# Kernel optimization log

Hardware: AMD Instinct MI355X
Metric: run time of the kernel (lower is better)

Reference implementation:

```python
import jax, jax.numpy as jnp
import numpy as np

V, E, H, C = 30000, 128, 256, 9  # vocab, embed dim, lstm hidden, num tags
B, S = 64, 512


def setup_inputs() -> dict:
    key = jax.random.key(0)
    ks = jax.random.split(key, 16)
    rn = lambda k, shape: jax.random.normal(k, shape, jnp.float32) * 0.1
    return {
        "token_ids": jax.random.randint(ks[0], (B, S), 0, V),
        "labels": jax.random.randint(ks[1], (B, S), 0, C),
        "attention_masks": jnp.ones((B, S), jnp.int32),
        "emb": rn(ks[2], (V, E)),
        # layer 0: input E; layer 1: input 2H. dim 0 = direction (fwd, bwd)
        "w_ih0": rn(ks[3], (2, 4 * H, E)),
        "w_hh0": rn(ks[4], (2, 4 * H, H)),
        "b_ih0": rn(ks[5], (2, 4 * H)),
        "b_hh0": rn(ks[6], (2, 4 * H)),
        "w_ih1": rn(ks[7], (2, 4 * H, 2 * H)),
        "w_hh1": rn(ks[8], (2, 4 * H, H)),
        "b_ih1": rn(ks[9], (2, 4 * H)),
        "b_hh1": rn(ks[10], (2, 4 * H)),
        "cls_w": rn(ks[11], (C, 2 * H)),
        "cls_b": rn(ks[12], (C,)),
        "start_trans": rn(ks[13], (C,)),
        "end_trans": rn(ks[14], (C,)),
        "trans": rn(ks[15], (C, C)),
    }


def _lstm_dir(x, w_ih, w_hh, b_ih, b_hh, reverse):
    # x: [B,S,in] -> [B,S,H]; gate order i,f,g,o as in torch
    Bq = x.shape[0]
    Hq = w_hh.shape[1]
    xg = jnp.einsum('bsi,gi->bsg', x, w_ih) + b_ih  # [B,S,4H]

    def step(carry, xg_t):
        h, c = carry
        g = xg_t + h @ w_hh.T + b_hh
        i, f, gg, o = jnp.split(g, 4, axis=-1)
        c = jax.nn.sigmoid(f) * c + jax.nn.sigmoid(i) * jnp.tanh(gg)
        h = jax.nn.sigmoid(o) * jnp.tanh(c)
        return (h, c), h

    init = (jnp.zeros((Bq, Hq), x.dtype), jnp.zeros((Bq, Hq), x.dtype))
    _, hs = jax.lax.scan(step, init, jnp.swapaxes(xg, 0, 1), reverse=reverse)
    return jnp.swapaxes(hs, 0, 1)


def _bilstm_layer(x, w_ih, w_hh, b_ih, b_hh):
    fwd = _lstm_dir(x, w_ih[0], w_hh[0], b_ih[0], b_hh[0], False)
    bwd = _lstm_dir(x, w_ih[1], w_hh[1], b_ih[1], b_hh[1], True)
    return jnp.concatenate([fwd, bwd], axis=-1)


def _crf_llh(em, tags, mask, start, end, trans):
    # torchcrf log-likelihood; em [B,S,C], tags [B,S], mask [B,S]
    m = mask.astype(em.dtype)
    em_tag = jnp.take_along_axis(em, tags[..., None], axis=2)[..., 0]  # [B,S]
    tr = trans[tags[:, :-1], tags[:, 1:]]  # [B,S-1]
    num = start[tags[:, 0]] + em_tag[:, 0] + jnp.sum(m[:, 1:] * (tr + em_tag[:, 1:]), axis=1)
    last_idx = jnp.sum(mask, axis=1).astype(jnp.int32) - 1
    last_tag = jnp.take_along_axis(tags, last_idx[:, None], axis=1)[:, 0]
    num = num + end[last_tag]

    alpha0 = start[None, :] + em[:, 0]  # [B,C]

    def step(alpha, xs):
        em_t, m_t = xs
        nxt = jax.nn.logsumexp(alpha[:, :, None] + trans[None] + em_t[:, None, :], axis=1)
        return jnp.where(m_t[:, None] > 0, nxt, alpha), None

    xs = (jnp.swapaxes(em[:, 1:], 0, 1), jnp.swapaxes(m[:, 1:], 0, 1))
    alpha, _ = jax.lax.scan(step, alpha0, xs)
    den = jax.nn.logsumexp(alpha + end[None, :], axis=1)
    return num - den


def _viterbi(em, mask, start, end, trans):
    Cq = em.shape[2]
    m = mask > 0
    score0 = start[None, :] + em[:, 0]
    idc = jnp.arange(Cq, dtype=jnp.int32)

    def step(score, xs):
        em_t, m_t = xs
        brd = score[:, :, None] + trans[None]  # [B,C_prev,C_next]
        best_prev = jnp.argmax(brd, axis=1).astype(jnp.int32)
        nxt = jnp.max(brd, axis=1) + em_t
        new = jnp.where(m_t[:, None], nxt, score)
        bp = jnp.where(m_t[:, None], best_prev, idc[None, :])  # self-pointer past seq end
        return new, bp

    xs = (jnp.swapaxes(em[:, 1:], 0, 1), jnp.swapaxes(m[:, 1:], 0, 1))
    score, hist = jax.lax.scan(step, score0, xs)  # hist: [S-1,B,C]
    last = jnp.argmax(score + end[None, :], axis=1).astype(jnp.int32)

    def back(tag, bp_t):
        prev = jnp.take_along_axis(bp_t, tag[:, None], axis=1)[:, 0]
        return prev, prev

    _, prevs = jax.lax.scan(back, last, hist, reverse=True)  # [S-1,B]
    return jnp.concatenate([jnp.swapaxes(prevs, 0, 1), last[:, None]], axis=1)  # [B,S]


def reference(token_ids, labels, attention_masks, emb, w_ih0, w_hh0, b_ih0, b_hh0,
              w_ih1, w_hh1, b_ih1, b_hh1, cls_w, cls_b, start_trans, end_trans, trans):
    x = emb[token_ids]  # [B,S,E]
    h = _bilstm_layer(x, w_ih0, w_hh0, b_ih0, b_hh0)  # [B,S,2H] (eval mode: no dropout)
    h = _bilstm_layer(h, w_ih1, w_hh1, b_ih1, b_hh1)
    emissions = h @ cls_w.T + cls_b  # [B,S,C]
    llh = _crf_llh(emissions, labels, attention_masks, start_trans, end_trans, trans)
    loss = -jnp.mean(llh)  # reduction='mean', negated
    tags = _viterbi(emissions, attention_masks, start_trans, end_trans, trans)
    return (loss, tags)
```

## Files before the change

kernel.cpp:

```cpp
#include <hip/hip_runtime.h>
#include <math.h>

#define BB 64
#define SS 512
#define HH 256
#define NC 9
#define G4 1024
#define TCLOG 7
#define TC 128
#define NCH (SS / TC)
#define VV 30000

#define KLQ 9

typedef _Float16 half2v __attribute__((ext_vector_type(2)));

__device__ __forceinline__ float sigf(float x) {
    return 1.0f / (1.0f + __expf(-x));
}
__device__ __forceinline__ float tanhfast(float x) {
    float a = fabsf(x);
    float e = __expf(-2.0f * a);
    float t = (1.0f - e) / (1.0f + e);
    return copysignf(t, x);
}
__device__ __forceinline__ int dot16q(uint4 w, uint4 h, int acc) {
    acc = __builtin_amdgcn_sdot4((int)w.x, (int)h.x, acc, false);
    acc = __builtin_amdgcn_sdot4((int)w.y, (int)h.y, acc, false);
    acc = __builtin_amdgcn_sdot4((int)w.z, (int)h.z, acc, false);
    acc = __builtin_amdgcn_sdot4((int)w.w, (int)h.w, acc, false);
    return acc;
}
__device__ __forceinline__ ushort f16b(float x) {
    return __builtin_bit_cast(ushort, (_Float16)x);
}

struct GJob {
    const unsigned char* A;
    const int*   tok;
    const unsigned char* W;
    const float* sw;
    const float* swA;
    const float* bias;
    ushort*      out;
    int tb, ts, is8, pad;
};
struct SJob {
    const ushort* xgF; const ushort* xgB;
    const uint*  wTq; const float* swf; const float* bhh2;
    ushort* hout; unsigned char* hout8; float* state;
    int doW8, tbF, tbB, doInit;
};
struct MegaP {
    SJob s;
    GJob g[4];
    int nScan, nGemm;
};

__device__ __forceinline__ int pad4(int r) { return r + (r >> 3); }

__device__ void gemm8_dev(unsigned char* sm, const GJob& G, int bx, int by) {
    uint4* As = (uint4*)sm;
    uint4* Bs = As + 144;
    const int tid = threadIdx.x;
    const int m0 = bx * 128, n0 = by * 128;
    const int lr = tid & 127;
    const int lpad = lr + (lr >> 3);
    const bool isA = tid < 128, isB = (tid >= 128 && tid < 256);
    const int tcc = (m0 + lr) & (TC - 1);
    const int bb  = (m0 + lr) >> TCLOG;
    const int tglob = G.tb + G.ts * tcc;
    const long arow = (long)bb * SS + tglob;
    const uint4* Ap = isA ? (const uint4*)(G.A + arow * 512) : nullptr;
    const uint4* Wp = isB ? (const uint4*)(G.W + (long)(n0 + lr) * 512) : nullptr;
    const int tr = tid >> 5, tn = tid & 31;

    int acc[4][4];
    #pragma unroll
    for (int i = 0; i < 4; i++)
        #pragma unroll
        for (int j = 0; j < 4; j++) acc[i][j] = 0;

    #pragma unroll 1
    for (int k0 = 0; k0 < 32; k0++) {
        if (isA) As[lpad] = Ap[k0];
        else if (isB) Bs[lpad] = Wp[k0];
        __syncthreads();
        uint4 a[4], w[4];
        #pragma unroll
        for (int i = 0; i < 4; i++) {
            a[i] = As[pad4(tr * 4 + i)];
            w[i] = Bs[pad4(tn * 4 + i)];
        }
        #pragma unroll
        for (int i = 0; i < 4; i++)
            #pragma unroll
            for (int j = 0; j < 4; j++)
                acc[i][j] = dot16q(w[j], a[i], acc[i][j]);
        __syncthreads();
    }

    #pragma unroll
    for (int i = 0; i < 4; i++) {
        ushort4 o;
        #pragma unroll
        for (int j = 0; j < 4; j++) {
            float r = fmaf((float)acc[i][j], G.sw[n0 + tn * 4 + j], G.bias[n0 + tn * 4 + j]);
            ((ushort*)&o)[j] = f16b(r);
        }
        *(ushort4*)(G.out + (long)(m0 + tr * 4 + i) * G4 + n0 + tn * 4) = o;
    }
}

__device__ void gemm8e_dev(unsigned char* sm, const GJob& G, int bx, int by) {
    uint4* As = (uint4*)sm;
    uint4* Bs = As + 144;
    const int tid = threadIdx.x;
    const int m0 = bx * 128, n0 = by * 128;
    const int lr = tid & 127;
    const int lpad = lr + (lr >> 3);
    const bool isA = tid < 128, isB = (tid >= 128 && tid < 256);
    const int tcc = (m0 + lr) & (TC - 1);
    const int bb  = (m0 + lr) >> TCLOG;
    const int tglob = G.tb + G.ts * tcc;
    const long arow = (long)bb * SS + tglob;
    const uint4* Ap = isA ? (const uint4*)(G.A + (long)G.tok[arow] * 128) : nullptr;
    const uint4* Wp = isB ? (const uint4*)(G.W + (long)(n0 + lr) * 128) : nullptr;
    const int tr = tid >> 5, tn = tid & 31;

    int acc[4][4];
    #pragma unroll
    for (int i = 0; i < 4; i++)
        #pragma unroll
        for (int j = 0; j < 4; j++) acc[i][j] = 0;

    #pragma unroll 1
    for (int k0 = 0; k0 < 8; k0++) {
        if (isA) As[lpad] = Ap[k0];
        else if (isB) Bs[lpad] = Wp[k0];
        __syncthreads();
        uint4 a[4], w[4];
        #pragma unroll
        for (int i = 0; i < 4; i++) {
            a[i] = As[pad4(tr * 4 + i)];
            w[i] = Bs[pad4(tn * 4 + i)];
        }
        #pragma unroll
        for (int i = 0; i < 4; i++)
            #pragma unroll
            for (int j = 0; j < 4; j++)
                acc[i][j] = dot16q(w[j], a[i], acc[i][j]);
        __syncthreads();
    }

    float sA[4];
    #pragma unroll
    for (int i = 0; i < 4; i++) {
        const int m = m0 + tr * 4 + i;
        const int tcc_i = m & (TC - 1);
        const int bb_i  = m >> TCLOG;
        const long ar = (long)bb_i * SS + G.tb + G.ts * tcc_i;
        sA[i] = G.swA[G.tok[ar]];
    }
    float sW[4], bs[4];
    #pragma unroll
    for (int j = 0; j < 4; j++) {
        sW[j] = G.sw[n0 + tn * 4 + j];
        bs[j] = G.bias[n0 + tn * 4 + j];
    }
    #pragma unroll
    for (int i = 0; i < 4; i++) {
        ushort4 o;
        #pragma unroll
        for (int j = 0; j < 4; j++) {
            float r = fmaf((float)acc[i][j] * sA[i], sW[j], bs[j]);
            ((ushort*)&o)[j] = f16b(r);
        }
        *(ushort4*)(G.out + (long)(m0 + tr * 4 + i) * G4 + n0 + tn * 4) = o;
    }
}

__device__ void scan_dev(unsigned char* sm, const SJob& S, int b, int d) {
    const int j = threadIdx.x;
    const ushort* xg = (d ? S.xgB : S.xgF) + (long)b * TC * G4 + j;
    const uint4* wTd = (const uint4*)S.wTq + (long)d * 16 * 1024;

    uint4* lwq = (uint4*)sm;
    float* gl  = (float*)(sm + 147456);
    uint*  hq  = (uint*)(sm + 147456 + 4096);

    #pragma unroll
    for (int kc = 0; kc < KLQ; kc++)
        lwq[kc * 1024 + j] = wTd[(long)kc * 1024 + j];

    const float bj  = S.bhh2[d * G4 + j];
    const float scl = S.swf[d * G4 + j];
    float c_reg = 0.f, h_reg = 0.f;
    if (j < HH) {
        if (!S.doInit) {
            h_reg = S.state[((d * BB + b) * 2 + 0) * HH + j];
            c_reg = S.state[((d * BB + b) * 2 + 1) * HH + j];
        }
        ((char*)hq)[j] = (char)__float2int_rn(h_reg * 127.f);
    }
    __syncthreads();

    #pragma unroll 1
    for (int tc = 0; tc < TC; ++tc) {
        const int rb = tc & 1;
        const uint4* hc = (const uint4*)(hq + rb * 64);
        int isum = 0;
        #pragma unroll
        for (int kc = 0; kc < KLQ; kc++)
            isum = dot16q(lwq[kc * 1024 + j], hc[kc], isum);
        #pragma unroll
        for (int kc = KLQ; kc < 16; kc++)
            isum = dot16q(wTd[(long)kc * 1024 + j], hc[kc], isum);

        float xv = (float)__builtin_bit_cast(_Float16, xg[(long)tc * G4]);
        gl[j] = fmaf((float)isum, scl, xv + bj);
        __syncthreads();
        if (j < HH) {
            float gi = gl[j], gf = gl[j + 256], gg = gl[j + 512], go = gl[j + 768];
            c_reg = sigf(gf) * c_reg + sigf(gi) * tanhfast(gg);
            float h = sigf(go) * tanhfast(c_reg);
            h_reg = h;
            int qh = __float2int_rn(h * 127.f);
            ((char*)(hq + (rb ^ 1) * 64))[j] = (char)qh;
            const int t = d ? (S.tbB - tc) : (S.tbF + tc);
            if (S.doW8) S.hout8[((long)(b * SS + t)) * 512 + d * HH + j] = (unsigned char)(char)qh;
            else        S.hout [((long)(b * SS + t)) * 512 + d * HH + j] = f16b(h);
        }
        __syncthreads();
    }

    if (j < HH) {
        S.state[((d * BB + b) * 2 + 0) * HH + j] = h_reg;
        S.state[((d * BB + b) * 2 + 1) * HH + j] = c_reg;
    }
}

__global__ __launch_bounds__(1024, 4) void mega(MegaP p) {
    __shared__ __align__(16) unsigned char sm[152064];
    const int blk = blockIdx.x;
    if (blk < p.nScan * 128) {
        const int local = blk & 127;
        scan_dev(sm, p.s, local & 63, local >> 6);
    } else {
        const int gb = blk - p.nScan * 128;
        const int job = gb >> 9, t = gb & 511;
        const GJob& G = p.g[job];
        if (G.is8 == 1) gemm8_dev(sm, G, t & 63, t >> 6);
        else            gemm8e_dev(sm, G, t & 63, t >> 6);
    }
}

__global__ void quant_whh(const float* __restrict__ whh, uint* __restrict__ wTq,
                          float* __restrict__ swf) {
    const int row = blockIdx.x;
    const int t = threadIdx.x;
    float4 v = *(const float4*)(whh + (long)row * 256 + t * 4);
    float mx = fmaxf(fmaxf(fabsf(v.x), fabsf(v.y)), fmaxf(fabsf(v.z), fabsf(v.w)));
    #pragma unroll
    for (int o = 32; o > 0; o >>= 1) mx = fmaxf(mx, __shfl_xor(mx, o));
    float inv = (mx > 0.f) ? 127.f / mx : 0.f;
    int q0 = (int)rintf(v.x * inv) & 255;
    int q1 = (int)rintf(v.y * inv) & 255;
    int q2 = (int)rintf(v.z * inv) & 255;
    int q3 = (int)rintf(v.w * inv) & 255;
    uint u = (uint)q0 | ((uint)q1 << 8) | ((uint)q2 << 16) | ((uint)q3 << 24);
    const int dir = row >> 10, j = row & 1023;
    const int kc = t >> 2, l4 = t & 3;
    wTq[(((long)(dir * 16 + kc) * 1024 + j) << 2) + l4] = u;
    if (t == 0) swf[row] = (mx > 0.f) ? (mx / 127.f) * (1.f / 127.f) : 0.f;
}

template <int NP>
__global__ void quant_rows(const float* __restrict__ in, unsigned char* __restrict__ out,
                           float* __restrict__ sc, int mode) {
    const int row = blockIdx.x;
    const int t = threadIdx.x;
    const int K = NP * 64;
    const float* src = in + (long)row * K + t * NP;
    float v[NP];
    float mx = 0.f;
    #pragma unroll
    for (int i = 0; i < NP; i++) { v[i] = src[i]; mx = fmaxf(mx, fabsf(v[i])); }
    #pragma unroll
    for (int o = 32; o > 0; o >>= 1) mx = fmaxf(mx, __shfl_xor(mx, o));
    float inv = (mx > 0.f) ? 127.f / mx : 0.f;
    unsigned char q[NP];
    #pragma unroll
    for (int i = 0; i < NP; i++) q[i] = (unsigned char)((int)rintf(v[i] * inv) & 255);
    unsigned char* dst = out + (long)row * K + t * NP;
    if (NP == 2) {
        *(ushort*)dst = *(ushort*)q;
    } else {
        *(uint*)dst = *(uint*)q;
        *(uint*)(dst + 4) = *(uint*)(q + 4);
    }
    if (t == 0) sc[row] = (mx <= 0.f) ? 0.f
                        : (mode == 0 ? mx / 127.f : mx / (127.f * 127.f));
}

__global__ __launch_bounds__(256) void emissions_k16(
    const ushort* __restrict__ h1, const float* __restrict__ clsw,
    const float* __restrict__ clsb, float* __restrict__ em)
{
    long u = (long)blockIdx.x * 256 + threadIdx.x;
    if (u >= (long)BB * SS * NC) return;
    int c = (int)(u % NC);
    long m = u / NC;
    const uint* hr = (const uint*)(h1 + m * 512);
    const float2* wr = (const float2*)(clsw + (long)c * 512);
    float s0 = 0, s1 = 0;
    #pragma unroll 8
    for (int q = 0; q < 256; q += 2) {
        half2v h0 = __builtin_bit_cast(half2v, hr[q]);
        half2v h1v = __builtin_bit_cast(half2v, hr[q + 1]);
        float2 w0 = wr[q], w1 = wr[q + 1];
        s0 += (float)h0.x * w0.x + (float)h0.y * w0.y;
        s1 += (float)h1v.x * w1.x + (float)h1v.y * w1.y;
    }
    em[u] = s0 + s1 + clsb[c];
}

__global__ __launch_bounds__(64) void crf_llh(
    const float* __restrict__ em, const int* __restrict__ labels,
    const int* __restrict__ mask, const float* __restrict__ start,
    const float* __restrict__ endt, const float* __restrict__ trans,
    float* __restrict__ llh)
{
    int b = blockIdx.x, j = threadIdx.x;
    bool act = j < NC;
    float tcol[NC];
    #pragma unroll
    for (int i = 0; i < NC; i++) tcol[i] = act ? trans[i * NC + j] : 0.f;
    const float* emb_ = em + (long)b * SS * NC;
    const int* lb = labels + b * SS;
    const int* mk = mask + b * SS;
    float alpha = act ? (start[j] + emb_[j]) : -1e30f;

    float num = 0.f;
    int msum = 0;
    for (int t = j; t < SS; t += 64) msum += (mk[t] != 0);
    for (int t = 1 + j; t < SS; t += 64) {
        float m = (float)mk[t];
        num += m * (trans[lb[t - 1] * NC + lb[t]] + emb_[t * NC + lb[t]]);
    }
    for (int o = 32; o > 0; o >>= 1) {
        num  += __shfl_down(num, o);
        msum += __shfl_down(msum, o);
    }
    msum = __shfl(msum, 0);

    for (int t = 1; t < SS; t++) {
        int m = mk[t];
        float emj = act ? emb_[t * NC + j] : 0.f;
        float v[NC];
        float mx = -1e30f;
        #pragma unroll
        for (int i = 0; i < NC; i++) {
            v[i] = __shfl(alpha, i) + tcol[i];
            mx = fmaxf(mx, v[i]);
        }
        float sum = 0.f;
        #pragma unroll
        for (int i = 0; i < NC; i++) sum += __expf(v[i] - mx);
        float nxt = mx + __logf(sum) + emj;
        if (m > 0 && act) alpha = nxt;
    }
    float fin = act ? alpha + endt[j] : -1e30f;
    float mx = -1e30f;
    #pragma unroll
    for (int i = 0; i < NC; i++) mx = fmaxf(mx, __shfl(fin, i));
    float s = 0.f;
    #pragma unroll
    for (int i = 0; i < NC; i++) s += __expf(__shfl(fin, i) - mx);
    float den = mx + __logf(s);
    if (j == 0) {
        int last_idx = msum - 1;
        float numer = num + start[lb[0]] + emb_[lb[0]] + endt[lb[last_idx]];
        llh[b] = numer - den;
    }
}

__global__ __launch_bounds__(64) void loss_k(const float* __restrict__ llh, float* __restrict__ out) {
    int j = threadIdx.x;
    float v = llh[j];
    for (int o = 32; o > 0; o >>= 1) v += __shfl_down(v, o);
    if (j == 0) out[0] = -v / 64.0f;
}

__global__ __launch_bounds__(64) void viterbi_k(
    const float* __restrict__ em, const int* __restrict__ mask,
    const float* __restrict__ start, const float* __restrict__ endt,
    const float* __restrict__ trans, float* __restrict__ outp)
{
    int b = blockIdx.x, j = threadIdx.x;
    bool act = j < NC;
    __shared__ unsigned char bp[SS][NC];
    float tcol[NC];
    #pragma unroll
    for (int i = 0; i < NC; i++) tcol[i] = act ? trans[i * NC + j] : 0.f;
    const float* emb_ = em + (long)b * SS * NC;
    const int* mk = mask + b * SS;
    float score = act ? (start[j] + emb_[j]) : -1e30f;

    for (int t = 1; t < SS; t++) {
        float best = 0.f;
        int bi = 0;
        #pragma unroll
        for (int i = 0; i < NC; i++) {
            float vv = __shfl(score, i) + tcol[i];
            if (i == 0 || vv > best) { best = vv; bi = i; }
        }
        int m = mk[t];
        float nxt = best + (act ? emb_[t * NC + j] : 0.f);
        if (act) {
            if (m > 0) { score = nxt; bp[t][j] = (unsigned char)bi; }
            else       { bp[t][j] = (unsigned char)j; }
        }
    }
    float fin = act ? score + endt[j] : -1e30f;
    float bestf = 0.f;
    int last = 0;
    #pragma unroll
    for (int i = 0; i < NC; i++) {
        float vv = __shfl(fin, i);
        if (i == 0 || vv > bestf) { bestf = vv; last = i; }
    }
    __syncthreads();
    if (j == 0) {
        int cur = last;
        outp[1 + (long)b * SS + (SS - 1)] = (float)cur;
        for (int t = SS - 1; t >= 1; t--) {
            cur = bp[t][cur];
            outp[1 + (long)b * SS + (t - 1)] = (float)cur;
        }
    }
}

extern "C" void kernel_launch(void* const* d_in, const int* in_sizes, int n_in,
                              void* d_out, int out_size, void* d_ws, size_t ws_size,
                              hipStream_t stream) {
    const int*   tok    = (const int*)d_in[0];
    const int*   lab    = (const int*)d_in[1];
    const int*   msk    = (const int*)d_in[2];
    const float* emb    = (const float*)d_in[3];
    const float* w_ih0  = (const float*)d_in[4];
    const float* w_hh0  = (const float*)d_in[5];
    const float* b_ih0  = (const float*)d_in[6];
    const float* b_hh0  = (const float*)d_in[7];
    const float* w_ih1  = (const float*)d_in[8];
    const float* w_hh1  = (const float*)d_in[9];
    const float* b_ih1  = (const float*)d_in[10];
    const float* b_hh1  = (const float*)d_in[11];
    const float* clsw   = (const float*)d_in[12];
    const float* clsb   = (const float*)d_in[13];
    const float* startt = (const float*)d_in[14];
    const float* endt   = (const float*)d_in[15];
    const float* transm = (const float*)d_in[16];
    float* out = (float*)d_out;

    size_t nH8  = (size_t)BB * SS * 512 / 4;
    size_t nHh  = (size_t)BB * SS * 512 / 2;
    size_t xgHalf = (size_t)BB * TC * G4;
    size_t nXGb = xgHalf * 2 / 2;
    size_t nWQ  = (size_t)2 * 16 * 1024 * 4;
    size_t nSW  = (size_t)2 * 1024;
    size_t nWQ1 = (size_t)2048 * 512 / 4;
    size_t nWQ0 = (size_t)2048 * 128 / 4;
    size_t nE8  = (size_t)VV * 128 / 4;
    size_t nEM  = (size_t)BB * SS * NC;
    size_t nST  = (size_t)2 * BB * 2 * HH;

    float* H08f = (float*)d_ws;
    float* H1f  = H08f + nH8;
    float* XG0a = H1f + nHh;
    float* XG0b = XG0a + nXGb;
    float* XG1a = XG0b + nXGb;
    float* XG1b = XG1a + nXGb;
    float* WQ0  = XG1b + nXGb;
    float* WQ1w = WQ0 + nWQ;
    float* SW0  = WQ1w + nWQ;
    float* SW1  = SW0 + nSW;
    float* WQI1 = SW1 + nSW;
    float* SWI1 = WQI1 + nWQ1;
    float* WQI0 = SWI1 + 2048;
    float* SWI0 = WQI0 + nWQ0;
    float* EMB8 = SWI0 + 2048;
    float* SA   = EMB8 + nE8;
    float* EM   = SA + VV;
    float* ST0  = EM + nEM;
    float* ST1  = ST0 + nST;
    float* LLH  = ST1 + nST;

    unsigned char* H08   = (unsigned char*)H08f;
    ushort*        H1h   = (ushort*)H1f;
    unsigned char* WQI1b = (unsigned char*)WQI1;
    unsigned char* WQI0b = (unsigned char*)WQI0;
    unsigned char* EMB8b = (unsigned char*)EMB8;
    ushort* XG0[2] = {(ushort*)XG0a, (ushort*)XG0b};
    ushort* XG1[2] = {(ushort*)XG1a, (ushort*)XG1b};

    quant_whh<<<2048, 64, 0, stream>>>(w_hh0, (uint*)WQ0, SW0);
    quant_whh<<<2048, 64, 0, stream>>>(w_hh1, (uint*)WQ1w, SW1);
    quant_rows<8><<<2048, 64, 0, stream>>>(w_ih1, WQI1b, SWI1, 1);
    quant_rows<2><<<2048, 64, 0, stream>>>(w_ih0, WQI0b, SWI0, 0);
    quant_rows<2><<<VV, 64, 0, stream>>>(emb, EMB8b, SA, 0);

    auto g0 = [&](int c, int dd) {
        GJob g{};
        g.A = EMB8b; g.tok = tok;
        g.W = WQI0b + (size_t)dd * 1024 * 128;
        g.sw = SWI0 + dd * 1024; g.swA = SA; g.bias = b_ih0 + dd * 1024;
        g.out = XG0[c & 1] + (size_t)dd * xgHalf;
        g.tb = dd ? (SS - 1 - c * TC) : (c * TC);
        g.ts = dd ? -1 : 1;
        g.is8 = 2;
        return g;
    };
    auto g8 = [&](int c, int dd) {
        GJob g{};
        g.A = H08; g.tok = nullptr;
        g.W = WQI1b + (size_t)dd * 1024 * 512;
        g.sw = SWI1 + dd * 1024; g.swA = nullptr; g.bias = b_ih1 + dd * 1024;
        g.out = XG1[c & 1] + (size_t)dd * xgHalf;
        g.tb = dd ? (SS - 1 - c * TC) : (c * TC);
        g.ts = dd ? -1 : 1;
        g.is8 = 1;
        return g;
    };
    auto sj = [&](int layer, int c) {
        SJob s{};
        ushort* xgb = layer ? XG1[c & 1] : XG0[c & 1];
        s.xgF = xgb; s.xgB = xgb + xgHalf;
        s.wTq = (const uint*)(layer ? WQ1w : WQ0);
        s.swf = layer ? SW1 : SW0;
        s.bhh2 = layer ? b_hh1 : b_hh0;
        s.hout = H1h; s.hout8 = H08;
        s.doW8 = layer ? 0 : 1;
        s.state = layer ? ST1 : ST0;
        s.tbF = c * TC; s.tbB = SS - 1 - c * TC;
        s.doInit = (c == 0);
        return s;
    };
    auto launch = [&](int nS, SJob s, GJob* gj, int nG) {
        MegaP p{};
        p.s = s;
        for (int i = 0; i < nG; i++) p.g[i] = gj[i];
        p.nScan = nS; p.nGemm = nG;
        mega<<<nS * 128 + nG * 512, 1024, 0, stream>>>(p);
    };

    { GJob j2[2] = {g0(0, 0), g0(0, 1)};          launch(0, SJob{}, j2, 2); }
    { GJob j2[2] = {g0(1, 0), g0(1, 1)};          launch(1, sj(0, 0), j2, 2); }
    { GJob j2[2] = {g0(2, 0), g0(2, 1)};          launch(1, sj(0, 1), j2, 2); }
    { GJob j4[4] = {g0(3, 0), g0(3, 1), g8(0, 0), g8(0, 1)};
                                                   launch(1, sj(0, 2), j4, 4); }
    { GJob j2[2] = {g8(1, 0), g8(1, 1)};          launch(1, sj(0, 3), j2, 2); }
    {                                              launch(1, sj(1, 0), nullptr, 0); }
    { GJob j2[2] = {g8(2, 0), g8(2, 1)};          launch(1, sj(1, 1), j2, 2); }
    { GJob j2[2] = {g8(3, 0), g8(3, 1)};          launch(1, sj(1, 2), j2, 2); }
    {                                              launch(1, sj(1, 3), nullptr, 0); }

    emissions_k16<<<((BB * SS * NC) + 255) / 256, 256, 0, stream>>>(H1h, clsw, clsb, EM);
    crf_llh<<<BB, 64, 0, stream>>>(EM, lab, msk, startt, endt, transm, LLH);
    loss_k<<<1, 64, 0, stream>>>(LLH, out);
    viterbi_k<<<BB, 64, 0, stream>>>(EM, msk, startt, endt, transm, out);
}
```

Before: 2.042 ms.

## Replace chunked mega-kernel pipeline with whole-sequence GEMM then full LSTM scan

Removes the chunked schedule in which each mega-kernel launch overlapped one 128-step scan chunk with the input-projection GEMM for the next chunk. Instead, each layer now runs one full GEMM over all timesteps, followed by a single scan kernel covering all 512 steps, which drops the per-chunk state save and restore and the extra launches. The CRF likelihood and Viterbi kernels are merged into one launch with 2*BB blocks. The cost is that GEMM work no longer overlaps with the latency-bound scan, and a full-size gate buffer is needed.

```diff
diff --git a/kernel.cpp b/kernel.cpp
--- a/kernel.cpp
+++ b/kernel.cpp
@@ -6,9 +6,6 @@
 #define HH 256
 #define NC 9
 #define G4 1024
-#define TCLOG 7
-#define TC 128
-#define NCH (SS / TC)
 #define VV 30000
 
 #define KLQ 9
@@ -34,226 +31,7 @@
 __device__ __forceinline__ ushort f16b(float x) {
     return __builtin_bit_cast(ushort, (_Float16)x);
 }
-
-struct GJob {
-    const unsigned char* A;
-    const int*   tok;
-    const unsigned char* W;
-    const float* sw;
-    const float* swA;
-    const float* bias;
-    ushort*      out;
-    int tb, ts, is8, pad;
-};
-struct SJob {
-    const ushort* xgF; const ushort* xgB;
-    const uint*  wTq; const float* swf; const float* bhh2;
-    ushort* hout; unsigned char* hout8; float* state;
-    int doW8, tbF, tbB, doInit;
-};
-struct MegaP {
-    SJob s;
-    GJob g[4];
-    int nScan, nGemm;
-};
-
 __device__ __forceinline__ int pad4(int r) { return r + (r >> 3); }
-
-__device__ void gemm8_dev(unsigned char* sm, const GJob& G, int bx, int by) {
-    uint4* As = (uint4*)sm;
-    uint4* Bs = As + 144;
-    const int tid = threadIdx.x;
-    const int m0 = bx * 128, n0 = by * 128;
-    const int lr = tid & 127;
-    const int lpad = lr + (lr >> 3);
-    const bool isA = tid < 128, isB = (tid >= 128 && tid < 256);
-    const int tcc = (m0 + lr) & (TC - 1);
-    const int bb  = (m0 + lr) >> TCLOG;
-    const int tglob = G.tb + G.ts * tcc;
-    const long arow = (long)bb * SS + tglob;
-    const uint4* Ap = isA ? (const uint4*)(G.A + arow * 512) : nullptr;
-    const uint4* Wp = isB ? (const uint4*)(G.W + (long)(n0 + lr) * 512) : nullptr;
-    const int tr = tid >> 5, tn = tid & 31;
-
-    int acc[4][4];
-    #pragma unroll
-    for (int i = 0; i < 4; i++)
-        #pragma unroll
-        for (int j = 0; j < 4; j++) acc[i][j] = 0;
-
-    #pragma unroll 1
-    for (int k0 = 0; k0 < 32; k0++) {
-        if (isA) As[lpad] = Ap[k0];
-        else if (isB) Bs[lpad] = Wp[k0];
-        __syncthreads();
-        uint4 a[4], w[4];
-        #pragma unroll
-        for (int i = 0; i < 4; i++) {
-            a[i] = As[pad4(tr * 4 + i)];
-            w[i] = Bs[pad4(tn * 4 + i)];
-        }
-        #pragma unroll
-        for (int i = 0; i < 4; i++)
-            #pragma unroll
-            for (int j = 0; j < 4; j++)
-                acc[i][j] = dot16q(w[j], a[i], acc[i][j]);
-        __syncthreads();
-    }
-
-    #pragma unroll
-    for (int i = 0; i < 4; i++) {
-        ushort4 o;
-        #pragma unroll
-        for (int j = 0; j < 4; j++) {
-            float r = fmaf((float)acc[i][j], G.sw[n0 + tn * 4 + j], G.bias[n0 + tn * 4 + j]);
-            ((ushort*)&o)[j] = f16b(r);
-        }
-        *(ushort4*)(G.out + (long)(m0 + tr * 4 + i) * G4 + n0 + tn * 4) = o;
-    }
-}
-
-__device__ void gemm8e_dev(unsigned char* sm, const GJob& G, int bx, int by) {
-    uint4* As = (uint4*)sm;
-    uint4* Bs = As + 144;
-    const int tid = threadIdx.x;
-    const int m0 = bx * 128, n0 = by * 128;
-    const int lr = tid & 127;
-    const int lpad = lr + (lr >> 3);
-    const bool isA = tid < 128, isB = (tid >= 128 && tid < 256);
-    const int tcc = (m0 + lr) & (TC - 1);
-    const int bb  = (m0 + lr) >> TCLOG;
-    const int tglob = G.tb + G.ts * tcc;
-    const long arow = (long)bb * SS + tglob;
-    const uint4* Ap = isA ? (const uint4*)(G.A + (long)G.tok[arow] * 128) : nullptr;
-    const uint4* Wp = isB ? (const uint4*)(G.W + (long)(n0 + lr) * 128) : nullptr;
-    const int tr = tid >> 5, tn = tid & 31;
-
-    int acc[4][4];
-    #pragma unroll
-    for (int i = 0; i < 4; i++)
-        #pragma unroll
-        for (int j = 0; j < 4; j++) acc[i][j] = 0;
-
-    #pragma unroll 1
-    for (int k0 = 0; k0 < 8; k0++) {
-        if (isA) As[lpad] = Ap[k0];
-        else if (isB) Bs[lpad] = Wp[k0];
-        __syncthreads();
-        uint4 a[4], w[4];
-        #pragma unroll
-        for (int i = 0; i < 4; i++) {
-            a[i] = As[pad4(tr * 4 + i)];
-            w[i] = Bs[pad4(tn * 4 + i)];
-        }
-        #pragma unroll
-        for (int i = 0; i < 4; i++)
-            #pragma unroll
-            for (int j = 0; j < 4; j++)
-                acc[i][j] = dot16q(w[j], a[i], acc[i][j]);
-        __syncthreads();
-    }
-
-    float sA[4];
-    #pragma unroll
-    for (int i = 0; i < 4; i++) {
-        const int m = m0 + tr * 4 + i;
-        const int tcc_i = m & (TC - 1);
-        const int bb_i  = m >> TCLOG;
-        const long ar = (long)bb_i * SS + G.tb + G.ts * tcc_i;
-        sA[i] = G.swA[G.tok[ar]];
-    }
-    float sW[4], bs[4];
-    #pragma unroll
-    for (int j = 0; j < 4; j++) {
-        sW[j] = G.sw[n0 + tn * 4 + j];
-        bs[j] = G.bias[n0 + tn * 4 + j];
-    }
-    #pragma unroll
-    for (int i = 0; i < 4; i++) {
-        ushort4 o;
-        #pragma unroll
-        for (int j = 0; j < 4; j++) {
-            float r = fmaf((float)acc[i][j] * sA[i], sW[j], bs[j]);
-            ((ushort*)&o)[j] = f16b(r);
-        }
-        *(ushort4*)(G.out + (long)(m0 + tr * 4 + i) * G4 + n0 + tn * 4) = o;
-    }
-}
-
-__device__ void scan_dev(unsigned char* sm, const SJob& S, int b, int d) {
-    const int j = threadIdx.x;
-    const ushort* xg = (d ? S.xgB : S.xgF) + (long)b * TC * G4 + j;
-    const uint4* wTd = (const uint4*)S.wTq + (long)d * 16 * 1024;
-
-    uint4* lwq = (uint4*)sm;
-    float* gl  = (float*)(sm + 147456);
-    uint*  hq  = (uint*)(sm + 147456 + 4096);
-
-    #pragma unroll
-    for (int kc = 0; kc < KLQ; kc++)
-        lwq[kc * 1024 + j] = wTd[(long)kc * 1024 + j];
-
-    const float bj  = S.bhh2[d * G4 + j];
-    const float scl = S.swf[d * G4 + j];
-    float c_reg = 0.f, h_reg = 0.f;
-    if (j < HH) {
-        if (!S.doInit) {
-            h_reg = S.state[((d * BB + b) * 2 + 0) * HH + j];
-            c_reg = S.state[((d * BB + b) * 2 + 1) * HH + j];
-        }
-        ((char*)hq)[j] = (char)__float2int_rn(h_reg * 127.f);
-    }
-    __syncthreads();
-
-    #pragma unroll 1
-    for (int tc = 0; tc < TC; ++tc) {
-        const int rb = tc & 1;
-        const uint4* hc = (const uint4*)(hq + rb * 64);
-        int isum = 0;
-        #pragma unroll
-        for (int kc = 0; kc < KLQ; kc++)
-            isum = dot16q(lwq[kc * 1024 + j], hc[kc], isum);
-        #pragma unroll
-        for (int kc = KLQ; kc < 16; kc++)
-            isum = dot16q(wTd[(long)kc * 1024 + j], hc[kc], isum);
-
-        float xv = (float)__builtin_bit_cast(_Float16, xg[(long)tc * G4]);
-        gl[j] = fmaf((float)isum, scl, xv + bj);
-        __syncthreads();
-        if (j < HH) {
-            float gi = gl[j], gf = gl[j + 256], gg = gl[j + 512], go = gl[j + 768];
-            c_reg = sigf(gf) * c_reg + sigf(gi) * tanhfast(gg);
-            float h = sigf(go) * tanhfast(c_reg);
-            h_reg = h;
-            int qh = __float2int_rn(h * 127.f);
-            ((char*)(hq + (rb ^ 1) * 64))[j] = (char)qh;
-            const int t = d ? (S.tbB - tc) : (S.tbF + tc);
-            if (S.doW8) S.hout8[((long)(b * SS + t)) * 512 + d * HH + j] = (unsigned char)(char)qh;
-            else        S.hout [((long)(b * SS + t)) * 512 + d * HH + j] = f16b(h);
-        }
-        __syncthreads();
-    }
-
-    if (j < HH) {
-        S.state[((d * BB + b) * 2 + 0) * HH + j] = h_reg;
-        S.state[((d * BB + b) * 2 + 1) * HH + j] = c_reg;
-    }
-}
-
-__global__ __launch_bounds__(1024, 4) void mega(MegaP p) {
-    __shared__ __align__(16) unsigned char sm[152064];
-    const int blk = blockIdx.x;
-    if (blk < p.nScan * 128) {
-        const int local = blk & 127;
-        scan_dev(sm, p.s, local & 63, local >> 6);
-    } else {
-        const int gb = blk - p.nScan * 128;
-        const int job = gb >> 9, t = gb & 511;
-        const GJob& G = p.g[job];
-        if (G.is8 == 1) gemm8_dev(sm, G, t & 63, t >> 6);
-        else            gemm8e_dev(sm, G, t & 63, t >> 6);
-    }
-}
 
 __global__ void quant_whh(const float* __restrict__ whh, uint* __restrict__ wTq,
                           float* __restrict__ swf) {
@@ -301,6 +79,197 @@
     }
     if (t == 0) sc[row] = (mx <= 0.f) ? 0.f
                         : (mode == 0 ? mx / 127.f : mx / (127.f * 127.f));
+}
+
+__global__ __launch_bounds__(1024, 2) void gemm8e_k(
+    const unsigned char* __restrict__ A8,
+    const int* __restrict__ tok,
+    const unsigned char* __restrict__ Wq,
+    const float* __restrict__ sw,
+    const float* __restrict__ swA,
+    const float* __restrict__ bias,
+    ushort* __restrict__ xg)
+{
+    __shared__ uint4 As[144], Bs[144];
+    const int tid = threadIdx.x;
+    const int m0 = blockIdx.x * 128;
+    const int n0 = blockIdx.y * 128;
+    const int d  = blockIdx.z;
+    const unsigned char* W = Wq + (size_t)d * 1024 * 128;
+    const float* swd = sw + d * 1024;
+    const float* bd  = bias + d * 1024;
+    ushort* outd = xg + (size_t)d * BB * SS * G4;
+
+    const int lr = tid & 127;
+    const int lpad = lr + (lr >> 3);
+    const bool isA = tid < 128, isB = (tid >= 128 && tid < 256);
+    const uint4* Ap = isA ? (const uint4*)(A8 + (long)tok[m0 + lr] * 128) : nullptr;
+    const uint4* Wp = isB ? (const uint4*)(W + (long)(n0 + lr) * 128) : nullptr;
+    const int tr = tid >> 5, tn = tid & 31;
+
+    int acc[4][4];
+    #pragma unroll
+    for (int i = 0; i < 4; i++)
+        #pragma unroll
+        for (int j = 0; j < 4; j++) acc[i][j] = 0;
+
+    #pragma unroll 1
+    for (int k0 = 0; k0 < 8; k0++) {
+        if (isA) As[lpad] = Ap[k0];
+        else if (isB) Bs[lpad] = Wp[k0];
+        __syncthreads();
+        uint4 a[4], w[4];
+        #pragma unroll
+        for (int i = 0; i < 4; i++) {
+            a[i] = As[pad4(tr * 4 + i)];
+            w[i] = Bs[pad4(tn * 4 + i)];
+        }
+        #pragma unroll
+        for (int i = 0; i < 4; i++)
+            #pragma unroll
+            for (int j = 0; j < 4; j++)
+                acc[i][j] = dot16q(w[j], a[i], acc[i][j]);
+        __syncthreads();
+    }
+
+    float sA[4];
+    #pragma unroll
+    for (int i = 0; i < 4; i++) sA[i] = swA[tok[m0 + tr * 4 + i]];
+    float sW[4], bs[4];
+    #pragma unroll
+    for (int j = 0; j < 4; j++) {
+        sW[j] = swd[n0 + tn * 4 + j];
+        bs[j] = bd[n0 + tn * 4 + j];
+    }
+    #pragma unroll
+    for (int i = 0; i < 4; i++) {
+        ushort4 o;
+        #pragma unroll
+        for (int j = 0; j < 4; j++) {
+            float r = fmaf((float)acc[i][j] * sA[i], sW[j], bs[j]);
+            ((ushort*)&o)[j] = f16b(r);
+        }
+        *(ushort4*)(outd + (long)(m0 + tr * 4 + i) * G4 + n0 + tn * 4) = o;
+    }
+}
+
+__global__ __launch_bounds__(1024, 2) void gemm8_k(
+    const unsigned char* __restrict__ A8,
+    const unsigned char* __restrict__ Wq,
+    const float* __restrict__ sw,
+    const float* __restrict__ bias,
+    ushort* __restrict__ xg)
+{
+    __shared__ uint4 As[144], Bs[144];
+    const int tid = threadIdx.x;
+    const int m0 = blockIdx.x * 128;
+    const int n0 = blockIdx.y * 128;
+    const int d  = blockIdx.z;
+    const unsigned char* W = Wq + (size_t)d * 1024 * 512;
+    const float* swd = sw + d * 1024;
+    const float* bd  = bias + d * 1024;
+    ushort* outd = xg + (size_t)d * BB * SS * G4;
+
+    const int lr = tid & 127;
+    const int lpad = lr + (lr >> 3);
+    const bool isA = tid < 128, isB = (tid >= 128 && tid < 256);
+    const uint4* Ap = isA ? (const uint4*)(A8 + (long)(m0 + lr) * 512) : nullptr;
+    const uint4* Wp = isB ? (const uint4*)(W + (long)(n0 + lr) * 512) : nullptr;
+    const int tr = tid >> 5, tn = tid & 31;
+
+    int acc[4][4];
+    #pragma unroll
+    for (int i = 0; i < 4; i++)
+        #pragma unroll
+        for (int j = 0; j < 4; j++) acc[i][j] = 0;
+
+    #pragma unroll 1
+    for (int k0 = 0; k0 < 32; k0++) {
+        if (isA) As[lpad] = Ap[k0];
+        else if (isB) Bs[lpad] = Wp[k0];
+        __syncthreads();
+        uint4 a[4], w[4];
+        #pragma unroll
+        for (int i = 0; i < 4; i++) {
+            a[i] = As[pad4(tr * 4 + i)];
+            w[i] = Bs[pad4(tn * 4 + i)];
+        }
+        #pragma unroll
+        for (int i = 0; i < 4; i++)
+            #pragma unroll
+            for (int j = 0; j < 4; j++)
+                acc[i][j] = dot16q(w[j], a[i], acc[i][j]);
+        __syncthreads();
+    }
+
+    #pragma unroll
+    for (int i = 0; i < 4; i++) {
+        ushort4 o;
+        #pragma unroll
+        for (int j = 0; j < 4; j++) {
+            float r = fmaf((float)acc[i][j], swd[n0 + tn * 4 + j], bd[n0 + tn * 4 + j]);
+            ((ushort*)&o)[j] = f16b(r);
+        }
+        *(ushort4*)(outd + (long)(m0 + tr * 4 + i) * G4 + n0 + tn * 4) = o;
+    }
+}
+
+__global__ __launch_bounds__(1024, 4) void lstm_qscan(
+    const ushort* __restrict__ xg,
+    const uint* __restrict__ wTq,
+    const float* __restrict__ swf,
+    const float* __restrict__ bhh2,
+    ushort* __restrict__ hout,
+    unsigned char* __restrict__ hout8,
+    int doW8)
+{
+    const int b = blockIdx.x;
+    const int d = blockIdx.y;
+    const int j = threadIdx.x;
+    const ushort* xgd = xg + ((size_t)d * BB * SS + (size_t)b * SS) * G4 + j;
+    const uint4* wTd = (const uint4*)wTq + (long)d * 16 * 1024;
+
+    __shared__ __align__(16) uint hq[2][64];
+    __shared__ float gl[G4];
+    __shared__ uint4 lwq[KLQ * 1024];
+
+    #pragma unroll
+    for (int kc = 0; kc < KLQ; kc++)
+        lwq[kc * 1024 + j] = wTd[(long)kc * 1024 + j];
+
+    const float bj  = bhh2[d * G4 + j];
+    const float scl = swf[d * G4 + j];
+    float c_reg = 0.f;
+    if (j < HH) ((char*)hq[0])[j] = 0;
+    __syncthreads();
+
+    #pragma unroll 1
+    for (int tc = 0; tc < SS; ++tc) {
+        const int rb = tc & 1;
+        const int t = d ? (SS - 1 - tc) : tc;
+        const uint4* hc = (const uint4*)hq[rb];
+        int isum = 0;
+        #pragma unroll
+        for (int kc = 0; kc < KLQ; kc++)
+            isum = dot16q(lwq[kc * 1024 + j], hc[kc], isum);
+        #pragma unroll
+        for (int kc = KLQ; kc < 16; kc++)
+            isum = dot16q(wTd[(long)kc * 1024 + j], hc[kc], isum);
+
+        float xv = (float)__builtin_bit_cast(_Float16, xgd[(long)t * G4]);
+        gl[j] = fmaf((float)isum, scl, xv + bj);
+        __syncthreads();
+        if (j < HH) {
+            float gi = gl[j], gf = gl[j + 256], gg = gl[j + 512], go = gl[j + 768];
+            c_reg = sigf(gf) * c_reg + sigf(gi) * tanhfast(gg);
+            float h = sigf(go) * tanhfast(c_reg);
+            int qh = __float2int_rn(h * 127.f);
+            ((char*)hq[rb ^ 1])[j] = (char)qh;
+            if (doW8) hout8[((long)(b * SS + t)) * 512 + d * HH + j] = (unsigned char)(char)qh;
+            else      hout [((long)(b * SS + t)) * 512 + d * HH + j] = f16b(h);
+        }
+        __syncthreads();
+    }
 }
 
 __global__ __launch_bounds__(256) void emissions_k16(
@@ -325,63 +294,108 @@
     em[u] = s0 + s1 + clsb[c];
 }
 
-__global__ __launch_bounds__(64) void crf_llh(
+__global__ __launch_bounds__(64) void crfvit_k(
     const float* __restrict__ em, const int* __restrict__ labels,
     const int* __restrict__ mask, const float* __restrict__ start,
     const float* __restrict__ endt, const float* __restrict__ trans,
-    float* __restrict__ llh)
+    float* __restrict__ llh, float* __restrict__ outp)
 {
-    int b = blockIdx.x, j = threadIdx.x;
-    bool act = j < NC;
-    float tcol[NC];
-    #pragma unroll
-    for (int i = 0; i < NC; i++) tcol[i] = act ? trans[i * NC + j] : 0.f;
-    const float* emb_ = em + (long)b * SS * NC;
-    const int* lb = labels + b * SS;
-    const int* mk = mask + b * SS;
-    float alpha = act ? (start[j] + emb_[j]) : -1e30f;
-
-    float num = 0.f;
-    int msum = 0;
-    for (int t = j; t < SS; t += 64) msum += (mk[t] != 0);
-    for (int t = 1 + j; t < SS; t += 64) {
-        float m = (float)mk[t];
-        num += m * (trans[lb[t - 1] * NC + lb[t]] + emb_[t * NC + lb[t]]);
-    }
-    for (int o = 32; o > 0; o >>= 1) {
-        num  += __shfl_down(num, o);
-        msum += __shfl_down(msum, o);
-    }
-    msum = __shfl(msum, 0);
-
-    for (int t = 1; t < SS; t++) {
-        int m = mk[t];
-        float emj = act ? emb_[t * NC + j] : 0.f;
-        float v[NC];
+    __shared__ unsigned char bp[SS][NC];
+    const int j = threadIdx.x;
+    const bool act = j < NC;
+    if (blockIdx.x < BB) {
+        const int b = blockIdx.x;
+        float tcol[NC];
+        #pragma unroll
+        for (int i = 0; i < NC; i++) tcol[i] = act ? trans[i * NC + j] : 0.f;
+        const float* emb_ = em + (long)b * SS * NC;
+        const int* lb = labels + b * SS;
+        const int* mk = mask + b * SS;
+        float alpha = act ? (start[j] + emb_[j]) : -1e30f;
+
+        float num = 0.f;
+        int msum = 0;
+        for (int t = j; t < SS; t += 64) msum += (mk[t] != 0);
+        for (int t = 1 + j; t < SS; t += 64) {
+            float m = (float)mk[t];
+            num += m * (trans[lb[t - 1] * NC + lb[t]] + emb_[t * NC + lb[t]]);
+        }
+        for (int o = 32; o > 0; o >>= 1) {
+            num  += __shfl_down(num, o);
+            msum += __shfl_down(msum, o);
+        }
+        msum = __shfl(msum, 0);
+
+        for (int t = 1; t < SS; t++) {
+            int m = mk[t];
+            float emj = act ? emb_[t * NC + j] : 0.f;
+            float v[NC];
+            float mx = -1e30f;
+            #pragma unroll
+            for (int i = 0; i < NC; i++) {
+                v[i] = __shfl(alpha, i) + tcol[i];
+                mx = fmaxf(mx, v[i]);
+            }
+            float sum = 0.f;
+            #pragma unroll
+            for (int i = 0; i < NC; i++) sum += __expf(v[i] - mx);
+            float nxt = mx + __logf(sum) + emj;
+            if (m > 0 && act) alpha = nxt;
+        }
+        float fin = act ? alpha + endt[j] : -1e30f;
         float mx = -1e30f;
         #pragma unroll
+        for (int i = 0; i < NC; i++) mx = fmaxf(mx, __shfl(fin, i));
+        float s = 0.f;
+        #pragma unroll
+        for (int i = 0; i < NC; i++) s += __expf(__shfl(fin, i) - mx);
+        float den = mx + __logf(s);
+        if (j == 0) {
+            int last_idx = msum - 1;
+            float numer = num + start[lb[0]] + emb_[lb[0]] + endt[lb[last_idx]];
+            llh[b] = numer - den;
+        }
+    } else {
+        const int b = blockIdx.x - BB;
+        float tcol[NC];
+        #pragma unroll
+        for (int i = 0; i < NC; i++) tcol[i] = act ? trans[i * NC + j] : 0.f;
+        const float* emb_ = em + (long)b * SS * NC;
+        const int* mk = mask + b * SS;
+        float score = act ? (start[j] + emb_[j]) : -1e30f;
+
+        for (int t = 1; t < SS; t++) {
+            float best = 0.f;
+            int bi = 0;
+            #pragma unroll
+            for (int i = 0; i < NC; i++) {
+                float vv = __shfl(score, i) + tcol[i];
+                if (i == 0 || vv > best) { best = vv; bi = i; }
+            }
+            int m = mk[t];
+            float nxt = best + (act ? emb_[t * NC + j] : 0.f);
+            if (act) {
+                if (m > 0) { score = nxt; bp[t][j] = (unsigned char)bi; }
+                else       { bp[t][j] = (unsigned char)j; }
+            }
+        }
+        float fin = act ? score + endt[j] : -1e30f;
+        float bestf = 0.f;
+        int last = 0;
+        #pragma unroll
         for (int i = 0; i < NC; i++) {
-            v[i] = __shfl(alpha, i) + tcol[i];
-            mx = fmaxf(mx, v[i]);
-        }
-        float sum = 0.f;
-        #pragma unroll
-        for (int i = 0; i < NC; i++) sum += __expf(v[i] - mx);
-        float nxt = mx + __logf(sum) + emj;
-        if (m > 0 && act) alpha = nxt;
-    }
-    float fin = act ? alpha + endt[j] : -1e30f;
-    float mx = -1e30f;
-    #pragma unroll
-    for (int i = 0; i < NC; i++) mx = fmaxf(mx, __shfl(fin, i));
-    float s = 0.f;
-    #pragma unroll
-    for (int i = 0; i < NC; i++) s += __expf(__shfl(fin, i) - mx);
-    float den = mx + __logf(s);
-    if (j == 0) {
-        int last_idx = msum - 1;
-        float numer = num + start[lb[0]] + emb_[lb[0]] + endt[lb[last_idx]];
-        llh[b] = numer - den;
+            float vv = __shfl(fin, i);
+            if (i == 0 || vv > bestf) { bestf = vv; last = i; }
+        }
+        __syncthreads();
+        if (j == 0) {
+            int cur = last;
+            outp[1 + (long)b * SS + (SS - 1)] = (float)cur;
+            for (int t = SS - 1; t >= 1; t--) {
+                cur = bp[t][cur];
+                outp[1 + (long)b * SS + (t - 1)] = (float)cur;
+            }
+        }
     }
 }
 
@@ -390,55 +404,6 @@
     float v = llh[j];
     for (int o = 32; o > 0; o >>= 1) v += __shfl_down(v, o);
     if (j == 0) out[0] = -v / 64.0f;
-}
-
-__global__ __launch_bounds__(64) void viterbi_k(
-    const float* __restrict__ em, const int* __restrict__ mask,
-    const float* __restrict__ start, const float* __restrict__ endt,
-    const float* __restrict__ trans, float* __restrict__ outp)
-{
-    int b = blockIdx.x, j = threadIdx.x;
-    bool act = j < NC;
-    __shared__ unsigned char bp[SS][NC];
-    float tcol[NC];
-    #pragma unroll
-    for (int i = 0; i < NC; i++) tcol[i] = act ? trans[i * NC + j] : 0.f;
-    const float* emb_ = em + (long)b * SS * NC;
-    const int* mk = mask + b * SS;
-    float score = act ? (start[j] + emb_[j]) : -1e30f;
-
-    for (int t = 1; t < SS; t++) {
-        float best = 0.f;
-        int bi = 0;
-        #pragma unroll
-        for (int i = 0; i < NC; i++) {
-            float vv = __shfl(score, i) + tcol[i];
-            if (i == 0 || vv > best) { best = vv; bi = i; }
-        }
-        int m = mk[t];
-        float nxt = best + (act ? emb_[t * NC + j] : 0.f);
-        if (act) {
-            if (m > 0) { score = nxt; bp[t][j] = (unsigned char)bi; }
-            else       { bp[t][j] = (unsigned char)j; }
-        }
-    }
-    float fin = act ? score + endt[j] : -1e30f;
-    float bestf = 0.f;
-    int last = 0;
-    #pragma unroll
-    for (int i = 0; i < NC; i++) {
-        float vv = __shfl(fin, i);
-        if (i == 0 || vv > bestf) { bestf = vv; last = i; }
-    }
-    __syncthreads();
-    if (j == 0) {
-        int cur = last;
-        outp[1 + (long)b * SS + (SS - 1)] = (float)cur;
-        for (int t = SS - 1; t >= 1; t--) {
-            cur = bp[t][cur];
-            outp[1 + (long)b * SS + (t - 1)] = (float)cur;
-        }
-    }
 }
 
 extern "C" void kernel_launch(void* const* d_in, const int* in_sizes, int n_in,
@@ -465,23 +430,18 @@
 
     size_t nH8  = (size_t)BB * SS * 512 / 4;
     size_t nHh  = (size_t)BB * SS * 512 / 2;
-    size_t xgHalf = (size_t)BB * TC * G4;
-    size_t nXGb = xgHalf * 2 / 2;
+    size_t nXG  = (size_t)2 * BB * SS * G4 / 2;
     size_t nWQ  = (size_t)2 * 16 * 1024 * 4;
     size_t nSW  = (size_t)2 * 1024;
     size_t nWQ1 = (size_t)2048 * 512 / 4;
     size_t nWQ0 = (size_t)2048 * 128 / 4;
     size_t nE8  = (size_t)VV * 128 / 4;
     size_t nEM  = (size_t)BB * SS * NC;
-    size_t nST  = (size_t)2 * BB * 2 * HH;
 
     float* H08f = (float*)d_ws;
     float* H1f  = H08f + nH8;
-    float* XG0a = H1f + nHh;
-    float* XG0b = XG0a + nXGb;
-    float* XG1a = XG0b + nXGb;
-    float* XG1b = XG1a + nXGb;
-    float* WQ0  = XG1b + nXGb;
+    float* XGf  = H1f + nHh;
+    float* WQ0  = XGf + nXG;
     float* WQ1w = WQ0 + nWQ;
     float* SW0  = WQ1w + nWQ;
     float* SW1  = SW0 + nSW;
@@ -492,17 +452,14 @@
     float* EMB8 = SWI0 + 2048;
     float* SA   = EMB8 + nE8;
     float* EM   = SA + VV;
-    float* ST0  = EM + nEM;
-    float* ST1  = ST0 + nST;
-    float* LLH  = ST1 + nST;
+    float* LLH  = EM + nEM;
 
     unsigned char* H08   = (unsigned char*)H08f;
     ushort*        H1h   = (ushort*)H1f;
+    ushort*        XG    = (ushort*)XGf;
     unsigned char* WQI1b = (unsigned char*)WQI1;
     unsigned char* WQI0b = (unsigned char*)WQI0;
     unsigned char* EMB8b = (unsigned char*)EMB8;
-    ushort* XG0[2] = {(ushort*)XG0a, (ushort*)XG0b};
-    ushort* XG1[2] = {(ushort*)XG1a, (ushort*)XG1b};
 
     quant_whh<<<2048, 64, 0, stream>>>(w_hh0, (uint*)WQ0, SW0);
     quant_whh<<<2048, 64, 0, stream>>>(w_hh1, (uint*)WQ1w, SW1);
@@ -510,63 +467,15 @@
     quant_rows<2><<<2048, 64, 0, stream>>>(w_ih0, WQI0b, SWI0, 0);
     quant_rows<2><<<VV, 64, 0, stream>>>(emb, EMB8b, SA, 0);
 
-    auto g0 = [&](int c, int dd) {
-        GJob g{};
-        g.A = EMB8b; g.tok = tok;
-        g.W = WQI0b + (size_t)dd * 1024 * 128;
-        g.sw = SWI0 + dd * 1024; g.swA = SA; g.bias = b_ih0 + dd * 1024;
-        g.out = XG0[c & 1] + (size_t)dd * xgHalf;
-        g.tb = dd ? (SS - 1 - c * TC) : (c * TC);
-        g.ts = dd ? -1 : 1;
-        g.is8 = 2;
-        return g;
-    };
-    auto g8 = [&](int c, int dd) {
-        GJob g{};
-        g.A = H08; g.tok = nullptr;
-        g.W = WQI1b + (size_t)dd * 1024 * 512;
-        g.sw = SWI1 + dd * 1024; g.swA = nullptr; g.bias = b_ih1 + dd * 1024;
-        g.out = XG1[c & 1] + (size_t)dd * xgHalf;
-        g.tb = dd ? (SS - 1 - c * TC) : (c * TC);
-        g.ts = dd ? -1 : 1;
-        g.is8 = 1;
-        return g;
-    };
-    auto sj = [&](int layer, int c) {
-        SJob s{};
-        ushort* xgb = layer ? XG1[c & 1] : XG0[c & 1];
-        s.xgF = xgb; s.xgB = xgb + xgHalf;
-        s.wTq = (const uint*)(layer ? WQ1w : WQ0);
-        s.swf = layer ? SW1 : SW0;
-        s.bhh2 = layer ? b_hh1 : b_hh0;
-        s.hout = H1h; s.hout8 = H08;
-        s.doW8 = layer ? 0 : 1;
-        s.state = layer ? ST1 : ST0;
-        s.tbF = c * TC; s.tbB = SS - 1 - c * TC;
-        s.doInit = (c == 0);
-        return s;
-    };
-    auto launch = [&](int nS, SJob s, GJob* gj, int nG) {
-        MegaP p{};
-        p.s = s;
-        for (int i = 0; i < nG; i++) p.g[i] = gj[i];
-        p.nScan = nS; p.nGemm = nG;
-        mega<<<nS * 128 + nG * 512, 1024, 0, stream>>>(p);
-    };
-
-    { GJob j2[2] = {g0(0, 0), g0(0, 1)};          launch(0, SJob{}, j2, 2); }
-    { GJob j2[2] = {g0(1, 0), g0(1, 1)};          launch(1, sj(0, 0), j2, 2); }
-    { GJob j2[2] = {g0(2, 0), g0(2, 1)};          launch(1, sj(0, 1), j2, 2); }
-    { GJob j4[4] = {g0(3, 0), g0(3, 1), g8(0, 0), g8(0, 1)};
-                                                   launch(1, sj(0, 2), j4, 4); }
-    { GJob j2[2] = {g8(1, 0), g8(1, 1)};          launch(1, sj(0, 3), j2, 2); }
-    {                                              launch(1, sj(1, 0), nullptr, 0); }
-    { GJob j2[2] = {g8(2, 0), g8(2, 1)};          launch(1, sj(1, 1), j2, 2); }
-    { GJob j2[2] = {g8(3, 0), g8(3, 1)};          launch(1, sj(1, 2), j2, 2); }
-    {                                              launch(1, sj(1, 3), nullptr, 0); }
+    dim3 gg(BB * SS / 128, G4 / 128, 2);
+    dim3 rg(BB, 2);
+
+    gemm8e_k<<<gg, 1024, 0, stream>>>(EMB8b, tok, WQI0b, SWI0, SA, b_ih0, XG);
+    lstm_qscan<<<rg, 1024, 0, stream>>>(XG, (const uint*)WQ0, SW0, b_hh0, H1h, H08, 1);
+    gemm8_k<<<gg, 1024, 0, stream>>>(H08, WQI1b, SWI1, b_ih1, XG);
+    lstm_qscan<<<rg, 1024, 0, stream>>>(XG, (const uint*)WQ1w, SW1, b_hh1, H1h, H08, 0);
 
     emissions_k16<<<((BB * SS * NC) + 255) / 256, 256, 0, stream>>>(H1h, clsw, clsb, EM);
-    crf_llh<<<BB, 64, 0, stream>>>(EM, lab, msk, startt, endt, transm, LLH);
+    crfvit_k<<<2 * BB, 64, 0, stream>>>(EM, lab, msk, startt, endt, transm, LLH, out);
     loss_k<<<1, 64, 0, stream>>>(LLH, out);
-    viterbi_k<<<BB, 64, 0, stream>>>(EM, msk, startt, endt, transm, out);
-}
+}
```

New measurement: 1.914 ms. 6.3% less time.
